# Optimization experiments

Hardware: AMD Instinct MI355X
Metric: run time of the kernel (lower is better)

## Reference

```python
import jax, jax.numpy as jnp
import numpy as np
from jax.scipy.special import logsumexp

# K particles, J proposal candidates, N taxa, R merges done, T current subtrees,
# S sites, A alphabet, D embedding dim
K, J, N, R, T, S, A, D = 128, 4, 64, 32, 32, 256, 4, 64
PRIOR_BL = 0.1       # expected branch length under exponential prior
TEMPERATURE = 1.0


def _gather_nodes(arr, idx):
    # arr: (Z, t, ...); idx: (Z,) -> (Z, ...)  (per-row gather, gather_K)
    i = idx.reshape((-1,) + (1,) * (arr.ndim - 1))
    return jnp.take_along_axis(arr, i, axis=1)[:, 0]


def _replace_with_merged(arr, idx1, idx2, new_val):
    # remove nodes idx1, idx2 from each row (keeping order) and append merged node
    t = arr.shape[1]
    pos = jnp.arange(t)
    removed = (pos[None, :] == idx1[:, None]) | (pos[None, :] == idx2[:, None])
    order = jnp.argsort(removed.astype(jnp.int32), axis=1, stable=True)
    kept = order[:, : t - 2]
    ki = kept.reshape(kept.shape + (1,) * (arr.ndim - 2))
    kept_vals = jnp.take_along_axis(arr, ki, axis=1)
    return jnp.concatenate([kept_vals, new_val[:, None]], axis=1)


def _hash_tree(h1, h2):
    # order-invariant int32 hash combine (wraps on overflow, as intended)
    mn = jnp.minimum(h1, h2)
    mx = jnp.maximum(h1, h2)
    return (mn * 1000003 + mx) * 40503 + 2531011


def _q_matrix(emb_ZxD, W_q):
    # GTR-style rate matrix from merged-node embedding (site-independent decoder)
    logits = (emb_ZxD @ W_q).reshape(-1, A, A)
    off = jax.nn.softplus(logits) * (1.0 - jnp.eye(A, dtype=logits.dtype))
    return off - jnp.eye(A, dtype=logits.dtype) * off.sum(-1, keepdims=True)


def setup_inputs() -> dict:
    key = jax.random.key(0)
    ks = jax.random.split(key, 20)
    merge1_indexes_Kxr = jax.random.randint(ks[0], (K, R), 0, N).astype(jnp.int32)
    merge2_indexes_Kxr = jax.random.randint(ks[1], (K, R), 0, N).astype(jnp.int32)
    branch1_lengths_Kxr = jax.random.uniform(ks[2], (K, R)) * 0.2 + 1e-3
    branch2_lengths_Kxr = jax.random.uniform(ks[3], (K, R)) * 0.2 + 1e-3
    embeddings_KxrxD = jax.random.normal(ks[4], (K, R, D))
    # leaf counts per subtree, summing to N per particle
    lc_row = jnp.concatenate([jnp.full((T // 2,), 1, jnp.int32), jnp.full((T - T // 2,), 3, jnp.int32)])
    leaf_counts_Kxt = jnp.tile(lc_row[None], (K, 1))
    hashes_Kxt = jax.random.randint(ks[5], (K, T), 0, 2 ** 30).astype(jnp.int32)
    embeddings_KxtxD = jax.random.normal(ks[6], (K, T, D))
    log_felsensteins_KxtxSxA = -jax.random.uniform(ks[7], (K, T, S, A)) * 3.0
    log_pi_K = -jax.random.uniform(ks[8], (K,)) * 100.0
    indexes_K = jax.random.randint(ks[9], (K,), 0, K).astype(jnp.int32)
    # proposal outputs (stand-in for the learned proposal): idx1 != idx2
    idx1_KxJ = jax.random.randint(ks[10], (K, J), 0, T).astype(jnp.int32)
    off = jax.random.randint(ks[11], (K, J), 1, T).astype(jnp.int32)
    idx2_KxJ = (idx1_KxJ + off) % T
    branch1_KxJ = jax.random.uniform(ks[12], (K, J)) * 0.2 + 1e-3
    branch2_KxJ = jax.random.uniform(ks[13], (K, J)) * 0.2 + 1e-3
    embedding_KxJxD = jax.random.normal(ks[14], (K, J, D))
    log_v_plus_KxJ = jnp.full((K, J), np.log(T * (T - 1) / 2.0), jnp.float32)
    gumbel_KxJ = jax.random.gumbel(ks[15], (K, J))
    W_q = jax.random.normal(ks[16], (D, A * A)) * 0.05
    W_stat = jax.random.normal(ks[17], (D, A)) * 0.05
    vals = np.zeros(2 * N, dtype=np.float64)
    for i in range(2, 2 * N):
        vals[i] = vals[i - 2] + np.log(i)
    log_double_factorials_2N = jnp.asarray(vals, jnp.float32)
    return {
        'indexes_K': indexes_K,
        'merge1_indexes_Kxr': merge1_indexes_Kxr,
        'merge2_indexes_Kxr': merge2_indexes_Kxr,
        'branch1_lengths_Kxr': branch1_lengths_Kxr,
        'branch2_lengths_Kxr': branch2_lengths_Kxr,
        'embeddings_KxrxD': embeddings_KxrxD,
        'leaf_counts_Kxt': leaf_counts_Kxt,
        'hashes_Kxt': hashes_Kxt,
        'embeddings_KxtxD': embeddings_KxtxD,
        'log_felsensteins_KxtxSxA': log_felsensteins_KxtxSxA,
        'log_pi_K': log_pi_K,
        'idx1_KxJ': idx1_KxJ,
        'idx2_KxJ': idx2_KxJ,
        'branch1_KxJ': branch1_KxJ,
        'branch2_KxJ': branch2_KxJ,
        'embedding_KxJxD': embedding_KxJxD,
        'log_v_plus_KxJ': log_v_plus_KxJ,
        'gumbel_KxJ': gumbel_KxJ,
        'W_q': W_q,
        'W_stat': W_stat,
        'log_double_factorials_2N': log_double_factorials_2N,
    }


def reference(indexes_K, merge1_indexes_Kxr, merge2_indexes_Kxr,
              branch1_lengths_Kxr, branch2_lengths_Kxr, embeddings_KxrxD,
              leaf_counts_Kxt, hashes_Kxt, embeddings_KxtxD,
              log_felsensteins_KxtxSxA, log_pi_K,
              idx1_KxJ, idx2_KxJ, branch1_KxJ, branch2_KxJ,
              embedding_KxJxD, log_v_plus_KxJ, gumbel_KxJ,
              W_q, W_stat, log_double_factorials_2N):
    # ---- ancestor resampling gather (ms[...][indexes_K]) ----
    g = lambda a: a[indexes_K]
    merge1_Kxr = g(merge1_indexes_Kxr); merge2_Kxr = g(merge2_indexes_Kxr)
    b1_Kxr = g(branch1_lengths_Kxr); b2_Kxr = g(branch2_lengths_Kxr)
    emb_KxrxD = g(embeddings_KxrxD)
    lc_Kxt = g(leaf_counts_Kxt); h_Kxt = g(hashes_Kxt)
    emb_KxtxD = g(embeddings_KxtxD)
    lf_KxtxSxA = g(log_felsensteins_KxtxSxA)
    logpi_K = g(log_pi_K)
    # ---- flatten proposal to Z = K*J (hash_trick=False: Z = K*J, no dedup) ----
    Z = K * J
    rep = lambda a: jnp.repeat(a, J, axis=0)  # K_to_Z
    idx1_Z = idx1_KxJ.reshape(Z); idx2_Z = idx2_KxJ.reshape(Z)
    branch1_Z = branch1_KxJ.reshape(Z); branch2_Z = branch2_KxJ.reshape(Z)
    emb_ZxD = embedding_KxJxD.reshape(Z, D)
    log_v_plus_Z = log_v_plus_KxJ.reshape(Z)
    merge1_Z = rep(merge1_Kxr); merge2_Z = rep(merge2_Kxr)
    b1_Z = rep(b1_Kxr); b2_Z = rep(b2_Kxr)
    embr_Z = rep(emb_KxrxD)
    lc_Z = rep(lc_Kxt); h_Z = rep(h_Kxt)
    embt_Z = rep(emb_KxtxD)
    lf_Z = rep(lf_KxtxSxA)
    logpi_Z = rep(logpi_K)
    # ---- append candidate branches ----
    b1_all = jnp.concatenate([b1_Z, branch1_Z[:, None]], axis=1)  # Z x (R+1)
    b2_all = jnp.concatenate([b2_Z, branch2_Z[:, None]], axis=1)
    # ---- merge step ----
    new_lc = _gather_nodes(lc_Z, idx1_Z) + _gather_nodes(lc_Z, idx2_Z)
    new_h = _hash_tree(_gather_nodes(h_Z, idx1_Z), _gather_nodes(h_Z, idx2_Z))
    lc_new = _replace_with_merged(lc_Z, idx1_Z, idx2_Z, new_lc)      # Z x (T-1)
    h_new = _replace_with_merged(h_Z, idx1_Z, idx2_Z, new_h)
    embt_new = _replace_with_merged(embt_Z, idx1_Z, idx2_Z, emb_ZxD)
    # ---- Felsenstein pruning update ----
    Q = _q_matrix(emb_ZxD, W_q)                                      # Z x A x A
    expm = jax.scipy.linalg.expm
    P1 = jax.vmap(expm)(Q * branch1_Z[:, None, None])
    P2 = jax.vmap(expm)(Q * branch2_Z[:, None, None])
    logP1 = jnp.log(jnp.clip(P1, 1e-30))
    logP2 = jnp.log(jnp.clip(P2, 1e-30))
    lf1 = _gather_nodes(lf_Z, idx1_Z)  # Z x S x A
    lf2 = _gather_nodes(lf_Z, idx2_Z)
    new_lf = (logsumexp(logP1[:, None, :, :] + lf1[:, :, None, :], axis=-1)
              + logsumexp(logP2[:, None, :, :] + lf2[:, :, None, :], axis=-1))
    lf_new = _replace_with_merged(lf_Z, idx1_Z, idx2_Z, new_lf)      # Z x (T-1) x S x A
    # ---- stationary probs per node & log pi ----
    log_stat = jax.nn.log_softmax(embt_new @ W_stat, axis=-1)        # Z x (T-1) x A
    ll_nodes = logsumexp(lf_new + log_stat[:, :, None, :], axis=-1).sum(-1)  # Z x (T-1)
    log_lik_Z = ll_nodes.sum(-1)
    rate = 1.0 / PRIOR_BL
    log_branch_prior = ((jnp.log(rate) - rate * b1_all).sum(-1)
                        + (jnp.log(rate) - rate * b2_all).sum(-1))
    df_idx = jnp.clip(2 * lc_new - 3, 0, 2 * N - 1)
    log_topo = -log_double_factorials_2N[df_idx].sum(-1)
    log_pi_new_Z = log_lik_Z + log_branch_prior + log_topo
    log_v_minus_Z = jnp.log(jnp.sum(lc_new > 1, axis=-1).astype(jnp.float32))
    # ---- weights & sub-resampling ----
    log_w_Z = log_pi_new_Z - logpi_Z + log_v_minus_Z - log_v_plus_Z
    log_w_KxJ = log_w_Z.reshape(K, J)
    log_weight_K = logsumexp(log_w_KxJ, axis=1) - jnp.log(float(J))
    sub_idx_K = jnp.argmax(log_w_KxJ / TEMPERATURE + gumbel_KxJ, axis=1)  # Gumbel-max = Categorical sample
    sel = jnp.arange(K) * J + sub_idx_K
    gs = lambda a: a[sel]
    merge1_out = jnp.concatenate([gs(merge1_Z), gs(idx1_Z)[:, None]], axis=1)
    merge2_out = jnp.concatenate([gs(merge2_Z), gs(idx2_Z)[:, None]], axis=1)
    embr_out = jnp.concatenate([gs(embr_Z), gs(emb_ZxD)[:, None, :]], axis=1)
    return (merge1_out, merge2_out, gs(b1_all), gs(b2_all), embr_out,
            gs(lc_new), gs(h_new), gs(embt_new), gs(lf_new),
            gs(log_pi_new_Z), log_weight_K, gs(log_lik_Z))
```

## Files before the change

### kernel.cpp

```cpp
#include <hip/hip_runtime.h>
#include <math.h>

constexpr int K_ = 128, J_ = 4, R_ = 32, T_ = 32, S_ = 256, A_ = 4, D_ = 64;
constexpr int Z_ = K_ * J_;
constexpr int NDF_ = 128;
constexpr float RATE_ = 10.0f;

constexpr int OFF_M1   = 0;
constexpr int OFF_M2   = OFF_M1 + K_ * 33;
constexpr int OFF_B1   = OFF_M2 + K_ * 33;
constexpr int OFF_B2   = OFF_B1 + K_ * 33;
constexpr int OFF_EMBR = OFF_B2 + K_ * 33;
constexpr int OFF_LC   = OFF_EMBR + K_ * 33 * D_;
constexpr int OFF_H    = OFF_LC + K_ * 31;
constexpr int OFF_EMBT = OFF_H + K_ * 31;
constexpr int OFF_LF   = OFF_EMBT + K_ * 31 * D_;
constexpr int OFF_LPN  = OFF_LF + K_ * 31 * S_ * A_;
constexpr int OFF_LW   = OFF_LPN + K_;
constexpr int OFF_LL   = OFF_LW + K_;


__device__ inline float lse4f(float a, float b, float c, float d) {
    float m = fmaxf(fmaxf(a, b), fmaxf(c, d));
    return m + logf(expf(a - m) + expf(b - m) + expf(c - m) + expf(d - m));
}

__global__ __launch_bounds__(256) void k_expm(
    const float* __restrict__ br1_KJ, const float* __restrict__ br2_KJ,
    const float* __restrict__ emb_KJD, const float* __restrict__ Wq,
    float* __restrict__ logP_ws ) {
    int tid = threadIdx.x;
    int g = tid >> 5;
    int q = tid & 31;
    int half = q >> 4;
    int e = q & 15;
    int i = e >> 2, j = e & 3;
    int z = blockIdx.x * 8 + g;

    __shared__ double s_sp[8][16];
    __shared__ double s_asc[8][2][16];
    __shared__ double s_term[8][2][16];
    __shared__ double s_acc[8][2][16];

    if (half == 0) {
        const float* emb = &emb_KJD[z * D_];
        float lg = 0.f;
        for (int d = 0; d < D_; ++d) lg += emb[d] * Wq[d * 16 + e];
        double sp = 0.0;
        if (i != j) {
            double x = (double)lg;
            sp = (x > 30.0) ? x : log1p(exp(x));
        }
        s_sp[g][e] = sp;
    }
    __syncthreads();

    double qv;
    if (i == j)
        qv = -(s_sp[g][i * 4 + 0] + s_sp[g][i * 4 + 1] +
               s_sp[g][i * 4 + 2] + s_sp[g][i * 4 + 3]);
    else
        qv = s_sp[g][e];
    double br = (double)(half == 0 ? br1_KJ[z] : br2_KJ[z]);
    double asc = qv * br * (1.0 / 64.0);
    s_asc[g][half][e] = asc;
    double ident = (i == j) ? 1.0 : 0.0;
    s_term[g][half][e] = ident;
    double accv = ident;
    __syncthreads();

    const double inv_n[11] = {0.0, 1.0, 0.5, 1.0 / 3.0, 0.25, 0.2,
                              1.0 / 6.0, 1.0 / 7.0, 0.125, 1.0 / 9.0, 0.1};
#pragma unroll
    for (int n = 1; n <= 10; ++n) {
        double t = (s_term[g][half][i * 4 + 0] * s_asc[g][half][0 * 4 + j] +
                    s_term[g][half][i * 4 + 1] * s_asc[g][half][1 * 4 + j] +
                    s_term[g][half][i * 4 + 2] * s_asc[g][half][2 * 4 + j] +
                    s_term[g][half][i * 4 + 3] * s_asc[g][half][3 * 4 + j]) *
                   inv_n[n];
        __syncthreads();
        s_term[g][half][e] = t;
        accv += t;
        __syncthreads();
    }

    s_acc[g][half][e] = accv;
    __syncthreads();
#pragma unroll
    for (int sq = 0; sq < 6; ++sq) {
        double t = s_acc[g][half][i * 4 + 0] * s_acc[g][half][0 * 4 + j] +
                   s_acc[g][half][i * 4 + 1] * s_acc[g][half][1 * 4 + j] +
                   s_acc[g][half][i * 4 + 2] * s_acc[g][half][2 * 4 + j] +
                   s_acc[g][half][i * 4 + 3] * s_acc[g][half][3 * 4 + j];
        __syncthreads();
        s_acc[g][half][e] = t;
        __syncthreads();
    }

    double p = s_acc[g][half][e];
    if (p < 1e-30) p = 1e-30;
    logP_ws[z * 32 + half * 16 + e] = (float)log(p);
}

__global__ __launch_bounds__(256) void k_node_ll(
    const int* __restrict__ indexes, const float* __restrict__ embt,
    const float* __restrict__ Wstat, const float* __restrict__ lf,
    float* __restrict__ node_ll) {
    int kt = blockIdx.x;
    int k = kt / T_, t = kt % T_;
    int src = indexes[k];
    int tid = threadIdx.x, wave = tid >> 6, lane = tid & 63;
    __shared__ float s_logit[4];
    __shared__ double s_part[4];
    {
        float e = embt[(src * T_ + t) * D_ + lane];
        float v = e * Wstat[lane * A_ + wave];
        for (int o = 32; o > 0; o >>= 1) v += __shfl_down(v, o, 64);
        if (lane == 0) s_logit[wave] = v;
    }
    __syncthreads();
    float l0 = s_logit[0], l1 = s_logit[1], l2 = s_logit[2], l3 = s_logit[3];
    float lse = lse4f(l0, l1, l2, l3);
    float ls0 = l0 - lse, ls1 = l1 - lse, ls2 = l2 - lse, ls3 = l3 - lse;
    const float4 f = *(const float4*)&lf[((size_t)(src * T_ + t) * S_ + tid) * A_];
    float site = lse4f(f.x + ls0, f.y + ls1, f.z + ls2, f.w + ls3);
    double v = (double)site;
    for (int o = 32; o > 0; o >>= 1) v += __shfl_down(v, o, 64);
    if (lane == 0) s_part[wave] = v;
    __syncthreads();
    if (tid == 0)
        node_ll[k * T_ + t] = (float)(s_part[0] + s_part[1] + s_part[2] + s_part[3]);
}

__global__ __launch_bounds__(256) void k_hyp(
    const int* __restrict__ indexes, const int* __restrict__ idx1_KJ,
    const int* __restrict__ idx2_KJ, const float* __restrict__ emb_KJD,
    const float* __restrict__ Wstat, const float* __restrict__ lf,
    const float* __restrict__ logP_ws, float* __restrict__ new_node_ll) {
    int z = blockIdx.x;
    int k = z / J_;
    int src = indexes[k];
    int i1 = idx1_KJ[z], i2 = idx2_KJ[z];
    int tid = threadIdx.x, wave = tid >> 6, lane = tid & 63;
    __shared__ float s_logP[32], s_logit[4];
    __shared__ double s_part[4];
    {
        float e = emb_KJD[z * D_ + lane];
        float v = e * Wstat[lane * A_ + wave];
        for (int o = 32; o > 0; o >>= 1) v += __shfl_down(v, o, 64);
        if (lane == 0) s_logit[wave] = v;
    }
    if (tid < 32) s_logP[tid] = logP_ws[z * 32 + tid];
    __syncthreads();
    float l0 = s_logit[0], l1 = s_logit[1], l2 = s_logit[2], l3 = s_logit[3];
    float lse = lse4f(l0, l1, l2, l3);
    float ls[4] = {l0 - lse, l1 - lse, l2 - lse, l3 - lse};
    const float4 f1 = *(const float4*)&lf[((size_t)(src * T_ + i1) * S_ + tid) * A_];
    const float4 f2 = *(const float4*)&lf[((size_t)(src * T_ + i2) * S_ + tid) * A_];
    float nlf[4];
#pragma unroll
    for (int a = 0; a < 4; ++a) {
        float t1 = lse4f(s_logP[a * 4 + 0] + f1.x, s_logP[a * 4 + 1] + f1.y,
                         s_logP[a * 4 + 2] + f1.z, s_logP[a * 4 + 3] + f1.w);
        float t2 = lse4f(s_logP[16 + a * 4 + 0] + f2.x, s_logP[16 + a * 4 + 1] + f2.y,
                         s_logP[16 + a * 4 + 2] + f2.z, s_logP[16 + a * 4 + 3] + f2.w);
        nlf[a] = t1 + t2;
    }
    float site = lse4f(nlf[0] + ls[0], nlf[1] + ls[1], nlf[2] + ls[2], nlf[3] + ls[3]);
    double v = (double)site;
    for (int o = 32; o > 0; o >>= 1) v += __shfl_down(v, o, 64);
    if (lane == 0) s_part[wave] = v;
    __syncthreads();
    if (tid == 0)
        new_node_ll[z] = (float)(s_part[0] + s_part[1] + s_part[2] + s_part[3]);
}

__global__ __launch_bounds__(64) void k_finalize(
    const int* __restrict__ indexes, const int* __restrict__ lc_Kt,
    const float* __restrict__ b1_Kr, const float* __restrict__ b2_Kr,
    const float* __restrict__ logpi_K, const int* __restrict__ idx1_KJ,
    const int* __restrict__ idx2_KJ, const float* __restrict__ br1_KJ,
    const float* __restrict__ br2_KJ, const float* __restrict__ logvp_KJ,
    const float* __restrict__ gumbel_KJ, const float* __restrict__ ldf,
    const float* __restrict__ node_ll, const float* __restrict__ new_node_ll,
    float* __restrict__ out, int* __restrict__ sub_idx) {
    int k = blockIdx.x;
    int lane = threadIdx.x;
    int src = indexes[k];
    double nll = 0.0, topo = 0.0, sb1 = 0.0, sb2 = 0.0;
    int cnt = 0;
    if (lane < T_) {
        nll = (double)node_ll[k * T_ + lane];
        int lc = lc_Kt[src * T_ + lane];
        int di = 2 * lc - 3; di = max(0, min(NDF_ - 1, di));
        topo = (double)ldf[di];
        cnt = (lc > 1) ? 1 : 0;
        sb1 = (double)b1_Kr[src * R_ + lane];
        sb2 = (double)b2_Kr[src * R_ + lane];
    }
    for (int o = 32; o > 0; o >>= 1) {
        nll += __shfl_down(nll, o, 64);
        topo += __shfl_down(topo, o, 64);
        sb1 += __shfl_down(sb1, o, 64);
        sb2 += __shfl_down(sb2, o, 64);
        cnt += __shfl_down(cnt, o, 64);
    }
    if (lane == 0) {
        double total_ll = nll, base_topo = -topo;
        const double lr = log(10.0);
        double lw[4], lpn[4], llik[4];
        for (int j = 0; j < J_; ++j) {
            int z = k * J_ + j;
            int i1 = idx1_KJ[z], i2 = idx2_KJ[z];
            int lc1 = lc_Kt[src * T_ + i1], lc2 = lc_Kt[src * T_ + i2];
            int nlc = lc1 + lc2;
            double loglik = total_ll - (double)node_ll[k * T_ + i1]
                                     - (double)node_ll[k * T_ + i2]
                                     + (double)new_node_ll[z];
            double lbp = 66.0 * lr
                       - (double)RATE_ * (sb1 + (double)br1_KJ[z] + sb2 + (double)br2_KJ[z]);
            int d1 = max(0, min(NDF_ - 1, 2 * lc1 - 3));
            int d2 = max(0, min(NDF_ - 1, 2 * lc2 - 3));
            int dn = max(0, min(NDF_ - 1, 2 * nlc - 3));
            double lt = base_topo + (double)ldf[d1] + (double)ldf[d2] - (double)ldf[dn];
            int cntj = cnt - ((lc1 > 1) ? 1 : 0) - ((lc2 > 1) ? 1 : 0) + 1;
            double lvm = log((double)cntj);
            lpn[j] = loglik + lbp + lt;
            llik[j] = loglik;
            lw[j] = lpn[j] - (double)logpi_K[src] + lvm - (double)logvp_KJ[z];
        }
        double m = fmax(fmax(lw[0], lw[1]), fmax(lw[2], lw[3]));
        double ssum = exp(lw[0] - m) + exp(lw[1] - m) + exp(lw[2] - m) + exp(lw[3] - m);
        double logw = m + log(ssum) - log((double)J_);
        int best = 0;
        double bv = lw[0] + (double)gumbel_KJ[k * J_ + 0];
        for (int j = 1; j < J_; ++j) {
            double v = lw[j] + (double)gumbel_KJ[k * J_ + j];
            if (v > bv) { bv = v; best = j; }
        }
        out[OFF_LPN + k] = (float)lpn[best];
        out[OFF_LW + k] = (float)logw;
        out[OFF_LL + k] = (float)llik[best];
        sub_idx[k] = best;
    }
}

__global__ __launch_bounds__(256) void k_output(
    const int* __restrict__ indexes, const int* __restrict__ m1_Kr,
    const int* __restrict__ m2_Kr, const float* __restrict__ b1_Kr,
    const float* __restrict__ b2_Kr, const float* __restrict__ embr,
    const int* __restrict__ lc_Kt, const int* __restrict__ h_Kt,
    const float* __restrict__ embt, const float* __restrict__ lf,
    const int* __restrict__ idx1_KJ, const int* __restrict__ idx2_KJ,
    const float* __restrict__ br1_KJ, const float* __restrict__ br2_KJ,
    const float* __restrict__ emb_KJD, const float* __restrict__ logP_ws,
    const int* __restrict__ sub_idx, float* __restrict__ out) {
    int blk = blockIdx.x;
    int k = blk >> 5, part = blk & 31;
    int tid = threadIdx.x;
    int src = indexes[k];
    int sub = sub_idx[k];
    int z = k * J_ + sub;
    int i1 = idx1_KJ[z], i2 = idx2_KJ[z];
    int mn = min(i1, i2), mx = max(i1, i2);

    if (part < 30) {
        int st = part;
        if (st >= mn) ++st;
        if (st >= mx) ++st;
        const float4 v = *(const float4*)&lf[((size_t)(src * T_ + st) * S_ + tid) * A_];
        *(float4*)&out[OFF_LF + ((size_t)(k * 31 + part) * S_ + tid) * A_] = v;
    } else if (part == 30) {
        __shared__ float s_logP[32];
        if (tid < 32) s_logP[tid] = logP_ws[z * 32 + tid];
        __syncthreads();
        const float4 f1 = *(const float4*)&lf[((size_t)(src * T_ + i1) * S_ + tid) * A_];
        const float4 f2 = *(const float4*)&lf[((size_t)(src * T_ + i2) * S_ + tid) * A_];
        float4 o4;
        float nlf[4];
#pragma unroll
        for (int a = 0; a < 4; ++a) {
            float t1 = lse4f(s_logP[a * 4 + 0] + f1.x, s_logP[a * 4 + 1] + f1.y,
                             s_logP[a * 4 + 2] + f1.z, s_logP[a * 4 + 3] + f1.w);
            float t2 = lse4f(s_logP[16 + a * 4 + 0] + f2.x, s_logP[16 + a * 4 + 1] + f2.y,
                             s_logP[16 + a * 4 + 2] + f2.z, s_logP[16 + a * 4 + 3] + f2.w);
            nlf[a] = t1 + t2;
        }
        o4.x = nlf[0]; o4.y = nlf[1]; o4.z = nlf[2]; o4.w = nlf[3];
        *(float4*)&out[OFF_LF + ((size_t)(k * 31 + 30) * S_ + tid) * A_] = o4;
    } else {
        for (int i = tid; i < 33; i += 256) {
            float v1, v2, fb1, fb2;
            if (i < 32) {
                v1 = (float)m1_Kr[src * R_ + i];
                v2 = (float)m2_Kr[src * R_ + i];
                fb1 = b1_Kr[src * R_ + i];
                fb2 = b2_Kr[src * R_ + i];
            } else {
                v1 = (float)i1; v2 = (float)i2;
                fb1 = br1_KJ[z]; fb2 = br2_KJ[z];
            }
            out[OFF_M1 + k * 33 + i] = v1;
            out[OFF_M2 + k * 33 + i] = v2;
            out[OFF_B1 + k * 33 + i] = fb1;
            out[OFF_B2 + k * 33 + i] = fb2;
        }
        for (int i = tid; i < 33 * D_; i += 256) {
            int r = i >> 6, d = i & 63;
            float v = (r < 32) ? embr[(src * R_ + r) * D_ + d] : emb_KJD[z * D_ + d];
            out[OFF_EMBR + k * 33 * D_ + i] = v;
        }
        for (int i = tid; i < 31; i += 256) {
            int lcv, hv;
            if (i < 30) {
                int st = i;
                if (st >= mn) ++st;
                if (st >= mx) ++st;
                lcv = lc_Kt[src * T_ + st];
                hv = h_Kt[src * T_ + st];
            } else {
                lcv = lc_Kt[src * T_ + i1] + lc_Kt[src * T_ + i2];
                int h1 = h_Kt[src * T_ + i1], h2 = h_Kt[src * T_ + i2];
                int hmn = min(h1, h2), hmx = max(h1, h2);
                unsigned int u = ((unsigned int)hmn * 1000003u + (unsigned int)hmx) * 40503u
                                 + 2531011u;
                hv = (int)u;
            }
            out[OFF_LC + k * 31 + i] = (float)lcv;
            out[OFF_H + k * 31 + i] = (float)hv;
        }
        for (int i = tid; i < 31 * D_; i += 256) {
            int t = i >> 6, d = i & 63;
            float v;
            if (t < 30) {
                int st = t;
                if (st >= mn) ++st;
                if (st >= mx) ++st;
                v = embt[(src * T_ + st) * D_ + d];
            } else {
                v = emb_KJD[z * D_ + d];
            }
            out[OFF_EMBT + k * 31 * D_ + i] = v;
        }
    }
}

extern "C" void kernel_launch(void* const* d_in, const int* in_sizes, int n_in,
                              void* d_out, int out_size, void* d_ws, size_t ws_size,
                              hipStream_t stream) {
    const int* indexes   = (const int*)d_in[0];
    const int* m1_Kr     = (const int*)d_in[1];
    const int* m2_Kr     = (const int*)d_in[2];
    const float* b1_Kr   = (const float*)d_in[3];
    const float* b2_Kr   = (const float*)d_in[4];
    const float* embr    = (const float*)d_in[5];
    const int* lc_Kt     = (const int*)d_in[6];
    const int* h_Kt      = (const int*)d_in[7];
    const float* embt    = (const float*)d_in[8];
    const float* lf      = (const float*)d_in[9];
    const float* logpi_K = (const float*)d_in[10];
    const int* idx1_KJ   = (const int*)d_in[11];
    const int* idx2_KJ   = (const int*)d_in[12];
    const float* br1_KJ  = (const float*)d_in[13];
    const float* br2_KJ  = (const float*)d_in[14];
    const float* emb_KJD = (const float*)d_in[15];
    const float* logvp_KJ = (const float*)d_in[16];
    const float* gumbel_KJ = (const float*)d_in[17];
    const float* Wq      = (const float*)d_in[18];
    const float* Wstat   = (const float*)d_in[19];
    const float* ldf     = (const float*)d_in[20];

    float* out = (float*)d_out;
    float* ws_f = (float*)d_ws;
    float* new_node_ll = ws_f;
    float* node_ll = ws_f + Z_;
    int* sub_idx = (int*)(ws_f + Z_ + K_ * T_);
    float* logP_ws = ws_f + Z_ + K_ * T_ + K_;

    k_expm<<<Z_ / 8, 256, 0, stream>>>(br1_KJ, br2_KJ, emb_KJD, Wq, logP_ws);
    k_node_ll<<<K_ * T_, 256, 0, stream>>>(indexes, embt, Wstat, lf, node_ll);
    k_hyp<<<Z_, 256, 0, stream>>>(indexes, idx1_KJ, idx2_KJ, emb_KJD, Wstat, lf,
                                  logP_ws, new_node_ll);
    k_finalize<<<K_, 64, 0, stream>>>(indexes, lc_Kt, b1_Kr, b2_Kr, logpi_K, idx1_KJ,
                                      idx2_KJ, br1_KJ, br2_KJ, logvp_KJ, gumbel_KJ,
                                      ldf, node_ll, new_node_ll, out, sub_idx);
    k_output<<<K_ * 32, 256, 0, stream>>>(indexes, m1_Kr, m2_Kr, b1_Kr, b2_Kr, embr,
                                          lc_Kt, h_Kt, embt, lf, idx1_KJ, idx2_KJ,
                                          br1_KJ, br2_KJ, emb_KJD, logP_ws, sub_idx, out);
}
```

Baseline: 149.2 us.

## Fuse expm, node and hypothesis likelihood kernels into one wave-per-item kernel

Merges the three launches (matrix exponential, per-node likelihood, merged-node likelihood) into one kernel whose blocks are split by index into node work and hypothesis work. Each wave now handles one item with 4 sites per lane, replacing block-wide shared-memory reductions with wave shuffles. The 4x4 expm runs per-row in registers with shuffles instead of shared memory and barriers. Fast __expf/__logf intrinsics replace the accurate versions. This removes two launch gaps and the logP round trip through global memory, at the cost of slightly lower precision and serial expm work on 8 lanes per hypothesis wave.

```diff
diff --git a/kernel.cpp b/kernel.cpp
--- a/kernel.cpp
+++ b/kernel.cpp
@@ -5,6 +5,9 @@
 constexpr int Z_ = K_ * J_;
 constexpr int NDF_ = 128;
 constexpr float RATE_ = 10.0f;
+
+constexpr int NB_NODE = K_ * T_ / 4;
+constexpr int NB_HYP  = Z_ / 4;
 
 constexpr int OFF_M1   = 0;
 constexpr int OFF_M2   = OFF_M1 + K_ * 33;
@@ -22,157 +25,159 @@
 
 __device__ inline float lse4f(float a, float b, float c, float d) {
     float m = fmaxf(fmaxf(a, b), fmaxf(c, d));
-    return m + logf(expf(a - m) + expf(b - m) + expf(c - m) + expf(d - m));
-}
-
-__global__ __launch_bounds__(256) void k_expm(
+    return m + __logf(__expf(a - m) + __expf(b - m) + __expf(c - m) + __expf(d - m));
+}
+
+__global__ __launch_bounds__(256) void k_main(
+    const int* __restrict__ indexes, const float* __restrict__ embt,
+    const float* __restrict__ Wstat, const float* __restrict__ lf,
+    const int* __restrict__ idx1_KJ, const int* __restrict__ idx2_KJ,
     const float* __restrict__ br1_KJ, const float* __restrict__ br2_KJ,
     const float* __restrict__ emb_KJD, const float* __restrict__ Wq,
-    float* __restrict__ logP_ws ) {
+    float* __restrict__ node_ll, float* __restrict__ new_node_ll,
+    float* __restrict__ logP_ws) {
+    int blk = blockIdx.x;
     int tid = threadIdx.x;
-    int g = tid >> 5;
-    int q = tid & 31;
-    int half = q >> 4;
-    int e = q & 15;
-    int i = e >> 2, j = e & 3;
-    int z = blockIdx.x * 8 + g;
-
-    __shared__ double s_sp[8][16];
-    __shared__ double s_asc[8][2][16];
-    __shared__ double s_term[8][2][16];
-    __shared__ double s_acc[8][2][16];
-
-    if (half == 0) {
+    int wave = tid >> 6, lane = tid & 63;
+
+    if (blk < NB_NODE) {
+        int kt = blk * 4 + wave;
+        int k = kt >> 5, t = kt & 31;
+        int src = indexes[k];
+        float e = embt[(src * T_ + t) * D_ + lane];
+        const float4 w4 = *(const float4*)&Wstat[lane * 4];
+        float g0 = e * w4.x, g1 = e * w4.y, g2 = e * w4.z, g3 = e * w4.w;
+#pragma unroll
+        for (int m = 32; m; m >>= 1) {
+            g0 += __shfl_xor(g0, m, 64);
+            g1 += __shfl_xor(g1, m, 64);
+            g2 += __shfl_xor(g2, m, 64);
+            g3 += __shfl_xor(g3, m, 64);
+        }
+        float lse = lse4f(g0, g1, g2, g3);
+        float ls0 = g0 - lse, ls1 = g1 - lse, ls2 = g2 - lse, ls3 = g3 - lse;
+        const float4* fr = (const float4*)&lf[((size_t)(src * T_ + t) * S_ + lane * 4) * A_];
+        double acc = 0.0;
+#pragma unroll
+        for (int s4 = 0; s4 < 4; ++s4) {
+            float4 f = fr[s4];
+            acc += (double)lse4f(f.x + ls0, f.y + ls1, f.z + ls2, f.w + ls3);
+        }
+#pragma unroll
+        for (int m = 32; m; m >>= 1) acc += __shfl_xor(acc, m, 64);
+        if (lane == 0) node_ll[kt] = (float)acc;
+    } else {
+        int z = (blk - NB_NODE) * 4 + wave;
+        int k = z >> 2;
+        int src = indexes[k];
+        int i1 = idx1_KJ[z], i2 = idx2_KJ[z];
+
+        __shared__ float s_val[4][20];
+        __shared__ float s_logP[4][32];
+
         const float* emb = &emb_KJD[z * D_];
-        float lg = 0.f;
-        for (int d = 0; d < D_; ++d) lg += emb[d] * Wq[d * 16 + e];
-        double sp = 0.0;
-        if (i != j) {
-            double x = (double)lg;
-            sp = (x > 30.0) ? x : log1p(exp(x));
-        }
-        s_sp[g][e] = sp;
-    }
-    __syncthreads();
-
-    double qv;
-    if (i == j)
-        qv = -(s_sp[g][i * 4 + 0] + s_sp[g][i * 4 + 1] +
-               s_sp[g][i * 4 + 2] + s_sp[g][i * 4 + 3]);
-    else
-        qv = s_sp[g][e];
-    double br = (double)(half == 0 ? br1_KJ[z] : br2_KJ[z]);
-    double asc = qv * br * (1.0 / 64.0);
-    s_asc[g][half][e] = asc;
-    double ident = (i == j) ? 1.0 : 0.0;
-    s_term[g][half][e] = ident;
-    double accv = ident;
-    __syncthreads();
-
-    const double inv_n[11] = {0.0, 1.0, 0.5, 1.0 / 3.0, 0.25, 0.2,
-                              1.0 / 6.0, 1.0 / 7.0, 0.125, 1.0 / 9.0, 0.1};
-#pragma unroll
-    for (int n = 1; n <= 10; ++n) {
-        double t = (s_term[g][half][i * 4 + 0] * s_asc[g][half][0 * 4 + j] +
-                    s_term[g][half][i * 4 + 1] * s_asc[g][half][1 * 4 + j] +
-                    s_term[g][half][i * 4 + 2] * s_asc[g][half][2 * 4 + j] +
-                    s_term[g][half][i * 4 + 3] * s_asc[g][half][3 * 4 + j]) *
-                   inv_n[n];
+        if (lane < 16) {
+            float lg = 0.f;
+            for (int d = 0; d < D_; ++d) lg += emb[d] * Wq[d * 16 + lane];
+            s_val[wave][lane] = lg;
+        } else if (lane < 20) {
+            int a = lane - 16;
+            float lg = 0.f;
+            for (int d = 0; d < D_; ++d) lg += emb[d] * Wstat[d * 4 + a];
+            s_val[wave][lane] = lg;
+        }
         __syncthreads();
-        s_term[g][half][e] = t;
-        accv += t;
+
+        if (lane < 8) {
+            int h = lane >> 2, r = lane & 3;
+            int base = h * 4;
+            double q[16];
+#pragma unroll
+            for (int i = 0; i < 4; ++i) {
+                double rs = 0.0;
+#pragma unroll
+                for (int j = 0; j < 4; ++j) {
+                    if (i != j) {
+                        double x = (double)s_val[wave][i * 4 + j];
+                        double sp = (x > 30.0) ? x : log1p(exp(x));
+                        q[i * 4 + j] = sp;
+                        rs += sp;
+                    }
+                }
+                q[i * 4 + i] = -rs;
+            }
+            double br = (double)(h == 0 ? br1_KJ[z] : br2_KJ[z]);
+            double c = br * (1.0 / 64.0);
+#pragma unroll
+            for (int e2 = 0; e2 < 16; ++e2) q[e2] *= c;
+            double trow[4], arow[4];
+#pragma unroll
+            for (int j = 0; j < 4; ++j) { trow[j] = (j == r) ? 1.0 : 0.0; arow[j] = trow[j]; }
+            const double inv_n[11] = {0.0, 1.0, 0.5, 1.0 / 3.0, 0.25, 0.2,
+                                      1.0 / 6.0, 1.0 / 7.0, 0.125, 1.0 / 9.0, 0.1};
+#pragma unroll
+            for (int n = 1; n <= 10; ++n) {
+                double nt[4];
+#pragma unroll
+                for (int j = 0; j < 4; ++j)
+                    nt[j] = (trow[0] * q[0 * 4 + j] + trow[1] * q[1 * 4 + j] +
+                             trow[2] * q[2 * 4 + j] + trow[3] * q[3 * 4 + j]) * inv_n[n];
+#pragma unroll
+                for (int j = 0; j < 4; ++j) { trow[j] = nt[j]; arow[j] += nt[j]; }
+            }
+#pragma unroll
+            for (int sq = 0; sq < 6; ++sq) {
+                double nrow[4];
+#pragma unroll
+                for (int j = 0; j < 4; ++j) {
+                    double aj = arow[j];
+                    nrow[j] = arow[0] * __shfl(aj, base + 0, 64)
+                            + arow[1] * __shfl(aj, base + 1, 64)
+                            + arow[2] * __shfl(aj, base + 2, 64)
+                            + arow[3] * __shfl(aj, base + 3, 64);
+                }
+#pragma unroll
+                for (int j = 0; j < 4; ++j) arow[j] = nrow[j];
+            }
+#pragma unroll
+            for (int j = 0; j < 4; ++j) {
+                float pf = (float)fmax(arow[j], 1e-30);
+                float lv = __logf(pf);
+                s_logP[wave][h * 16 + r * 4 + j] = lv;
+                logP_ws[z * 32 + h * 16 + r * 4 + j] = lv;
+            }
+        }
         __syncthreads();
-    }
-
-    s_acc[g][half][e] = accv;
-    __syncthreads();
-#pragma unroll
-    for (int sq = 0; sq < 6; ++sq) {
-        double t = s_acc[g][half][i * 4 + 0] * s_acc[g][half][0 * 4 + j] +
-                   s_acc[g][half][i * 4 + 1] * s_acc[g][half][1 * 4 + j] +
-                   s_acc[g][half][i * 4 + 2] * s_acc[g][half][2 * 4 + j] +
-                   s_acc[g][half][i * 4 + 3] * s_acc[g][half][3 * 4 + j];
-        __syncthreads();
-        s_acc[g][half][e] = t;
-        __syncthreads();
-    }
-
-    double p = s_acc[g][half][e];
-    if (p < 1e-30) p = 1e-30;
-    logP_ws[z * 32 + half * 16 + e] = (float)log(p);
-}
-
-__global__ __launch_bounds__(256) void k_node_ll(
-    const int* __restrict__ indexes, const float* __restrict__ embt,
-    const float* __restrict__ Wstat, const float* __restrict__ lf,
-    float* __restrict__ node_ll) {
-    int kt = blockIdx.x;
-    int k = kt / T_, t = kt % T_;
-    int src = indexes[k];
-    int tid = threadIdx.x, wave = tid >> 6, lane = tid & 63;
-    __shared__ float s_logit[4];
-    __shared__ double s_part[4];
-    {
-        float e = embt[(src * T_ + t) * D_ + lane];
-        float v = e * Wstat[lane * A_ + wave];
-        for (int o = 32; o > 0; o >>= 1) v += __shfl_down(v, o, 64);
-        if (lane == 0) s_logit[wave] = v;
-    }
-    __syncthreads();
-    float l0 = s_logit[0], l1 = s_logit[1], l2 = s_logit[2], l3 = s_logit[3];
-    float lse = lse4f(l0, l1, l2, l3);
-    float ls0 = l0 - lse, ls1 = l1 - lse, ls2 = l2 - lse, ls3 = l3 - lse;
-    const float4 f = *(const float4*)&lf[((size_t)(src * T_ + t) * S_ + tid) * A_];
-    float site = lse4f(f.x + ls0, f.y + ls1, f.z + ls2, f.w + ls3);
-    double v = (double)site;
-    for (int o = 32; o > 0; o >>= 1) v += __shfl_down(v, o, 64);
-    if (lane == 0) s_part[wave] = v;
-    __syncthreads();
-    if (tid == 0)
-        node_ll[k * T_ + t] = (float)(s_part[0] + s_part[1] + s_part[2] + s_part[3]);
-}
-
-__global__ __launch_bounds__(256) void k_hyp(
-    const int* __restrict__ indexes, const int* __restrict__ idx1_KJ,
-    const int* __restrict__ idx2_KJ, const float* __restrict__ emb_KJD,
-    const float* __restrict__ Wstat, const float* __restrict__ lf,
-    const float* __restrict__ logP_ws, float* __restrict__ new_node_ll) {
-    int z = blockIdx.x;
-    int k = z / J_;
-    int src = indexes[k];
-    int i1 = idx1_KJ[z], i2 = idx2_KJ[z];
-    int tid = threadIdx.x, wave = tid >> 6, lane = tid & 63;
-    __shared__ float s_logP[32], s_logit[4];
-    __shared__ double s_part[4];
-    {
-        float e = emb_KJD[z * D_ + lane];
-        float v = e * Wstat[lane * A_ + wave];
-        for (int o = 32; o > 0; o >>= 1) v += __shfl_down(v, o, 64);
-        if (lane == 0) s_logit[wave] = v;
-    }
-    if (tid < 32) s_logP[tid] = logP_ws[z * 32 + tid];
-    __syncthreads();
-    float l0 = s_logit[0], l1 = s_logit[1], l2 = s_logit[2], l3 = s_logit[3];
-    float lse = lse4f(l0, l1, l2, l3);
-    float ls[4] = {l0 - lse, l1 - lse, l2 - lse, l3 - lse};
-    const float4 f1 = *(const float4*)&lf[((size_t)(src * T_ + i1) * S_ + tid) * A_];
-    const float4 f2 = *(const float4*)&lf[((size_t)(src * T_ + i2) * S_ + tid) * A_];
-    float nlf[4];
-#pragma unroll
-    for (int a = 0; a < 4; ++a) {
-        float t1 = lse4f(s_logP[a * 4 + 0] + f1.x, s_logP[a * 4 + 1] + f1.y,
-                         s_logP[a * 4 + 2] + f1.z, s_logP[a * 4 + 3] + f1.w);
-        float t2 = lse4f(s_logP[16 + a * 4 + 0] + f2.x, s_logP[16 + a * 4 + 1] + f2.y,
-                         s_logP[16 + a * 4 + 2] + f2.z, s_logP[16 + a * 4 + 3] + f2.w);
-        nlf[a] = t1 + t2;
-    }
-    float site = lse4f(nlf[0] + ls[0], nlf[1] + ls[1], nlf[2] + ls[2], nlf[3] + ls[3]);
-    double v = (double)site;
-    for (int o = 32; o > 0; o >>= 1) v += __shfl_down(v, o, 64);
-    if (lane == 0) s_part[wave] = v;
-    __syncthreads();
-    if (tid == 0)
-        new_node_ll[z] = (float)(s_part[0] + s_part[1] + s_part[2] + s_part[3]);
+
+        float sl0 = s_val[wave][16], sl1 = s_val[wave][17];
+        float sl2 = s_val[wave][18], sl3 = s_val[wave][19];
+        float lseS = lse4f(sl0, sl1, sl2, sl3);
+        float ls0 = sl0 - lseS, ls1 = sl1 - lseS, ls2 = sl2 - lseS, ls3 = sl3 - lseS;
+        float p1[16], p2[16];
+#pragma unroll
+        for (int i = 0; i < 16; ++i) { p1[i] = s_logP[wave][i]; p2[i] = s_logP[wave][16 + i]; }
+        const float4* f1p = (const float4*)&lf[((size_t)(src * T_ + i1) * S_ + lane * 4) * A_];
+        const float4* f2p = (const float4*)&lf[((size_t)(src * T_ + i2) * S_ + lane * 4) * A_];
+        double acc = 0.0;
+#pragma unroll
+        for (int s4 = 0; s4 < 4; ++s4) {
+            float4 f = f1p[s4];
+            float4 g = f2p[s4];
+            float nlf[4];
+#pragma unroll
+            for (int a = 0; a < 4; ++a) {
+                float t1 = lse4f(p1[a * 4 + 0] + f.x, p1[a * 4 + 1] + f.y,
+                                 p1[a * 4 + 2] + f.z, p1[a * 4 + 3] + f.w);
+                float t2 = lse4f(p2[a * 4 + 0] + g.x, p2[a * 4 + 1] + g.y,
+                                 p2[a * 4 + 2] + g.z, p2[a * 4 + 3] + g.w);
+                nlf[a] = t1 + t2;
+            }
+            acc += (double)lse4f(nlf[0] + ls0, nlf[1] + ls1, nlf[2] + ls2, nlf[3] + ls3);
+        }
+#pragma unroll
+        for (int m = 32; m; m >>= 1) acc += __shfl_xor(acc, m, 64);
+        if (lane == 0) new_node_ll[z] = (float)acc;
+    }
 }
 
 __global__ __launch_bounds__(64) void k_finalize(
@@ -377,10 +382,9 @@
     int* sub_idx = (int*)(ws_f + Z_ + K_ * T_);
     float* logP_ws = ws_f + Z_ + K_ * T_ + K_;
 
-    k_expm<<<Z_ / 8, 256, 0, stream>>>(br1_KJ, br2_KJ, emb_KJD, Wq, logP_ws);
-    k_node_ll<<<K_ * T_, 256, 0, stream>>>(indexes, embt, Wstat, lf, node_ll);
-    k_hyp<<<Z_, 256, 0, stream>>>(indexes, idx1_KJ, idx2_KJ, emb_KJD, Wstat, lf,
-                                  logP_ws, new_node_ll);
+    k_main<<<NB_NODE + NB_HYP, 256, 0, stream>>>(
+        indexes, embt, Wstat, lf, idx1_KJ, idx2_KJ, br1_KJ, br2_KJ, emb_KJD, Wq,
+        node_ll, new_node_ll, logP_ws);
     k_finalize<<<K_, 64, 0, stream>>>(indexes, lc_Kt, b1_Kr, b2_Kr, logpi_K, idx1_KJ,
                                       idx2_KJ, br1_KJ, br2_KJ, logvp_KJ, gumbel_KJ,
                                       ldf, node_ll, new_node_ll, out, sub_idx);
```

Result: slower. 155.8 us (+4.4%).
